# Kernel optimization log

Hardware: AMD Instinct MI355X
Metric: run time of the kernel (lower is better)

Reference implementation:

```python
import jax, jax.numpy as jnp
import numpy as np

E, TOP_K = 8, 2          # num_experts, num_experts_per_tok
B, S, H, I = 4, 2048, 1024, 4096  # batch, seq, hidden, intermediate
STD = 0.02


def setup_inputs() -> dict:
    key = jax.random.key(0)
    k0, k1, k2, k3 = jax.random.split(key, 4)
    return {
        "x": jax.random.normal(k0, (B, S, H), jnp.float32),
        "w_gate": jax.random.normal(k1, (E, H), jnp.float32) * STD,                 # gate: Linear(H->E, no bias)
        "w_fc": jax.random.normal(k2, (E, I, H), jnp.float32) * STD,                # c_fc per-expert [E, out, in]
        "b_fc": jnp.zeros((E, I), jnp.float32),
        "w_proj": jax.random.normal(k3, (E, H, I), jnp.float32) * (STD / np.sqrt(2 * 24)),  # c_proj, n_layer=24 init scale
        "b_proj": jnp.zeros((E, H), jnp.float32),
    }


def reference(x, w_gate, w_fc, b_fc, w_proj, b_proj):
    b, s, h = x.shape
    xf = x.reshape(-1, h)                       # [T, H], T = B*S
    T = xf.shape[0]

    # --- routing (softmax in fp32, top-k, renormalize) ---
    router_logits = xf @ w_gate.T               # [T, E]
    probs = jax.nn.softmax(router_logits.astype(jnp.float32), axis=-1)
    top_w, top_idx = jax.lax.top_k(probs, TOP_K)            # [T, K]
    top_w = top_w / jnp.sum(top_w, axis=-1, keepdims=True)  # normalize_expert_weights
    top_w = top_w.astype(x.dtype)

    # combine[t, e] = gate weight of expert e for token t (0 if not selected)
    combine = jnp.zeros((T, E), x.dtype).at[jnp.arange(T)[:, None], top_idx].add(top_w)

    # --- experts: weighted sum of per-expert MLPs (same math as sort/gather/scatter) ---
    out = jnp.zeros_like(xf)
    for e in range(E):
        ht = jax.nn.gelu(xf @ w_fc[e].T + b_fc[e], approximate=False)  # [T, I]
        ht = ht @ w_proj[e].T + b_proj[e]                              # [T, H]
        out = out + combine[:, e:e + 1] * ht

    return out.reshape(b, s, h), router_logits
```

## Files before the change

kernel.cpp:

```cpp
#include <hip/hip_runtime.h>
#include <hip/hip_bf16.h>
#include <math.h>

#define T_TOK 8192
#define HID 1024
#define IDIM 4096
#define NE 8
#define TK (T_TOK*2)

typedef __attribute__((ext_vector_type(8))) short short8;
typedef __attribute__((ext_vector_type(4))) float f32x4;

__global__ __launch_bounds__(256) void cvt_kernel(const float* __restrict__ src,
                                                  __hip_bfloat16* __restrict__ dst, int n4)
{
    int i = blockIdx.x * 256 + threadIdx.x;
    int stride = gridDim.x * 256;
    for (; i < n4; i += stride) {
        float4 v = ((const float4*)src)[i];
        union { __hip_bfloat16 h[4]; ushort4 u; } t;
        t.h[0] = __float2bfloat16(v.x);
        t.h[1] = __float2bfloat16(v.y);
        t.h[2] = __float2bfloat16(v.z);
        t.h[3] = __float2bfloat16(v.w);
        ((ushort4*)dst)[i] = t.u;
    }
}

__global__ __launch_bounds__(64) void router_kernel(const float* __restrict__ x,
                                                    const float* __restrict__ wg,
                                                    float* __restrict__ logits_out,
                                                    int* __restrict__ top_idx,
                                                    float* __restrict__ top_w,
                                                    int* __restrict__ counts)
{
    int t = blockIdx.x;
    int lane = threadIdx.x;
    const float* xr = x + (size_t)t * HID;
    float acc[NE];
#pragma unroll
    for (int e = 0; e < NE; e++) acc[e] = 0.f;
    for (int h = lane; h < HID; h += 64) {
        float xv = xr[h];
#pragma unroll
        for (int e = 0; e < NE; e++) acc[e] += xv * wg[e * HID + h];
    }
#pragma unroll
    for (int e = 0; e < NE; e++)
        for (int off = 32; off > 0; off >>= 1)
            acc[e] += __shfl_down(acc[e], off, 64);
    if (lane == 0) {
        float mx = acc[0];
        for (int e = 1; e < NE; e++) mx = fmaxf(mx, acc[e]);
        float p[NE]; float s = 0.f;
        for (int e = 0; e < NE; e++) { p[e] = expf(acc[e] - mx); s += p[e]; }
        for (int e = 0; e < NE; e++) logits_out[(size_t)t * NE + e] = acc[e];
        int i1 = 0;
        for (int e = 1; e < NE; e++) if (p[e] > p[i1]) i1 = e;
        int i2 = -1;
        for (int e = 0; e < NE; e++) { if (e == i1) continue; if (i2 < 0 || p[e] > p[i2]) i2 = e; }
        float w1 = p[i1], w2 = p[i2], sw = w1 + w2;
        top_idx[t * 2] = i1; top_idx[t * 2 + 1] = i2;
        top_w[t * 2] = w1 / sw; top_w[t * 2 + 1] = w2 / sw;
        atomicAdd(&counts[i1], 1);
        atomicAdd(&counts[i2], 1);
    }
}

__global__ void scan_kernel(const int* __restrict__ counts, int* __restrict__ offsets)
{
    if (threadIdx.x == 0) {
        int s = 0;
        for (int e = 0; e < NE; e++) { offsets[e] = s; s += counts[e]; }
        offsets[NE] = s;
    }
}

__global__ __launch_bounds__(256) void scatter_kernel(const int* __restrict__ top_idx,
                                                      const float* __restrict__ top_w,
                                                      const int* __restrict__ offsets,
                                                      int* __restrict__ counts2,
                                                      int* __restrict__ expert_tok,
                                                      float* __restrict__ slot_w,
                                                      int* __restrict__ slot_of)
{
    int t = blockIdx.x * 256 + threadIdx.x;
    if (t >= T_TOK) return;
    for (int k = 0; k < 2; k++) {
        int e = top_idx[t * 2 + k];
        int pos = atomicAdd(&counts2[e], 1);
        int slot = offsets[e] + pos;
        expert_tok[slot] = t;
        slot_w[slot] = top_w[t * 2 + k];
        slot_of[t * 2 + k] = slot;
    }
}

__global__ __launch_bounds__(256) void gather_kernel(const float* __restrict__ x,
                                                     const int* __restrict__ expert_tok,
                                                     __hip_bfloat16* __restrict__ xg)
{
    int slot = blockIdx.x;
    int tok = expert_tok[slot];
    const float* src = x + (size_t)tok * HID;
    __hip_bfloat16* dst = xg + (size_t)slot * HID;
    for (int h = threadIdx.x; h < HID; h += 256)
        dst[h] = __float2bfloat16(src[h]);
}

#define LDS_STRIDE 40

template <int KDIM>
__device__ __forceinline__ void moe_gemm_loop(const __hip_bfloat16* __restrict__ A,
                                              int m0, int cnt,
                                              const __hip_bfloat16* __restrict__ B,
                                              __hip_bfloat16* Alds, __hip_bfloat16* Blds,
                                              f32x4 (&acc)[4][4])
{
    const int tid = threadIdx.x;
    const int lane = tid & 63, wave = tid >> 6;
    const int wm = (wave & 1) * 64, wn = (wave >> 1) * 64;
    const int fm = lane & 15, q = lane >> 4;

    for (int kt = 0; kt < KDIM / 32; ++kt) {
        const int k0 = kt * 32;
        __syncthreads();
#pragma unroll
        for (int i = 0; i < 2; i++) {
            int cid = tid + 256 * i;
            int r = cid >> 2, c = cid & 3;
            int ra = m0 + r; ra = (ra < cnt) ? ra : (cnt - 1);
            *(uint4*)&Alds[r * LDS_STRIDE + c * 8] =
                *(const uint4*)&A[(size_t)ra * KDIM + k0 + c * 8];
            *(uint4*)&Blds[r * LDS_STRIDE + c * 8] =
                *(const uint4*)&B[(size_t)r * KDIM + k0 + c * 8];
        }
        __syncthreads();
        short8 af[4], bfr[4];
#pragma unroll
        for (int mi = 0; mi < 4; mi++)
            af[mi] = *(const short8*)&Alds[(wm + mi * 16 + fm) * LDS_STRIDE + q * 8];
#pragma unroll
        for (int ni = 0; ni < 4; ni++)
            bfr[ni] = *(const short8*)&Blds[(wn + ni * 16 + fm) * LDS_STRIDE + q * 8];
#pragma unroll
        for (int mi = 0; mi < 4; mi++)
#pragma unroll
            for (int ni = 0; ni < 4; ni++)
                acc[mi][ni] = __builtin_amdgcn_mfma_f32_16x16x32_bf16(af[mi], bfr[ni],
                                                                      acc[mi][ni], 0, 0, 0);
    }
}

__global__ __launch_bounds__(256) void gemm_fc_kernel(const __hip_bfloat16* __restrict__ xg,
                                                      const __hip_bfloat16* __restrict__ wfc,
                                                      const float* __restrict__ b_fc,
                                                      const int* __restrict__ offsets,
                                                      __hip_bfloat16* __restrict__ ht)
{
    __shared__ __hip_bfloat16 Alds[128 * LDS_STRIDE];
    __shared__ __hip_bfloat16 Blds[128 * LDS_STRIDE];
    const int e = blockIdx.z;
    const int off = offsets[e];
    const int cnt = offsets[e + 1] - off;
    const int m0 = blockIdx.y * 128;
    if (m0 >= cnt) return;
    const int n0 = blockIdx.x * 128;

    f32x4 acc[4][4] = {};
    moe_gemm_loop<HID>(xg + (size_t)off * HID, m0, cnt,
                       wfc + (size_t)e * IDIM * HID + (size_t)n0 * HID, Alds, Blds, acc);

    const int tid = threadIdx.x, lane = tid & 63, wave = tid >> 6;
    const int wm = (wave & 1) * 64, wn = (wave >> 1) * 64, fm = lane & 15, q = lane >> 4;
#pragma unroll
    for (int ni = 0; ni < 4; ni++) {
        int n = n0 + wn + ni * 16 + fm;
        float bias = b_fc[(size_t)e * IDIM + n];
#pragma unroll
        for (int mi = 0; mi < 4; mi++) {
#pragma unroll
            for (int r = 0; r < 4; r++) {
                int m = m0 + wm + mi * 16 + q * 4 + r;
                if (m < cnt) {
                    float v = acc[mi][ni][r] + bias;
                    float g = 0.5f * v * (1.0f + erff(v * 0.70710678118654752f));
                    ht[(size_t)(off + m) * IDIM + n] = __float2bfloat16(g);
                }
            }
        }
    }
}

__global__ __launch_bounds__(256) void gemm_proj_kernel(const __hip_bfloat16* __restrict__ ht,
                                                        const __hip_bfloat16* __restrict__ wproj,
                                                        const float* __restrict__ b_proj,
                                                        const int* __restrict__ offsets,
                                                        const float* __restrict__ slot_w,
                                                        __hip_bfloat16* __restrict__ contrib)
{
    __shared__ __hip_bfloat16 Alds[128 * LDS_STRIDE];
    __shared__ __hip_bfloat16 Blds[128 * LDS_STRIDE];
    const int e = blockIdx.z;
    const int off = offsets[e];
    const int cnt = offsets[e + 1] - off;
    const int m0 = blockIdx.y * 128;
    if (m0 >= cnt) return;
    const int n0 = blockIdx.x * 128;

    f32x4 acc[4][4] = {};
    moe_gemm_loop<IDIM>(ht + (size_t)off * IDIM, m0, cnt,
                        wproj + (size_t)e * HID * IDIM + (size_t)n0 * IDIM, Alds, Blds, acc);

    const int tid = threadIdx.x, lane = tid & 63, wave = tid >> 6;
    const int wm = (wave & 1) * 64, wn = (wave >> 1) * 64, fm = lane & 15, q = lane >> 4;
#pragma unroll
    for (int mi = 0; mi < 4; mi++) {
#pragma unroll
        for (int r = 0; r < 4; r++) {
            int m = m0 + wm + mi * 16 + q * 4 + r;
            if (m >= cnt) continue;
            float sw = slot_w[off + m];
#pragma unroll
            for (int ni = 0; ni < 4; ni++) {
                int n = n0 + wn + ni * 16 + fm;
                float v = acc[mi][ni][r] + b_proj[(size_t)e * HID + n];
                contrib[(size_t)(off + m) * HID + n] = __float2bfloat16(v * sw);
            }
        }
    }
}

__global__ __launch_bounds__(256) void combine_kernel(const __hip_bfloat16* __restrict__ contrib,
                                                      const int* __restrict__ slot_of,
                                                      float* __restrict__ out)
{
    int t = blockIdx.x;
    int s0 = slot_of[t * 2], s1 = slot_of[t * 2 + 1];
    const __hip_bfloat16* c0 = contrib + (size_t)s0 * HID;
    const __hip_bfloat16* c1 = contrib + (size_t)s1 * HID;
    float* o = out + (size_t)t * HID;
    for (int h = threadIdx.x; h < HID; h += 256)
        o[h] = __bfloat162float(c0[h]) + __bfloat162float(c1[h]);
}

extern "C" void kernel_launch(void* const* d_in, const int* in_sizes, int n_in,
                              void* d_out, int out_size, void* d_ws, size_t ws_size,
                              hipStream_t stream)
{
    const float* x      = (const float*)d_in[0];
    const float* w_gate = (const float*)d_in[1];
    const float* w_fc   = (const float*)d_in[2];
    const float* b_fc   = (const float*)d_in[3];
    const float* w_proj = (const float*)d_in[4];
    const float* b_proj = (const float*)d_in[5];
    float* out = (float*)d_out;
    float* logits_out = out + (size_t)T_TOK * HID;

    char* ws = (char*)d_ws;
    const size_t WB = (size_t)NE * IDIM * HID * 2;
    size_t o_wfc     = 0;
    size_t o_wproj   = o_wfc + WB;
    size_t o_xg      = o_wproj + WB;
    size_t o_ht      = o_xg + (size_t)TK * HID * 2;
    size_t o_contrib = o_ht + (size_t)TK * IDIM * 2;
    size_t o_route   = o_contrib + (size_t)TK * HID * 2;

    __hip_bfloat16* wfc_b   = (__hip_bfloat16*)(ws + o_wfc);
    __hip_bfloat16* wproj_b = (__hip_bfloat16*)(ws + o_wproj);
    __hip_bfloat16* xg      = (__hip_bfloat16*)(ws + o_xg);
    __hip_bfloat16* ht      = (__hip_bfloat16*)(ws + o_ht);
    __hip_bfloat16* contrib = (__hip_bfloat16*)(ws + o_contrib);

    size_t ro = o_route;
    int*   top_idx    = (int*)(ws + ro);   ro += (size_t)T_TOK * 2 * 4;
    float* top_w      = (float*)(ws + ro); ro += (size_t)T_TOK * 2 * 4;
    int*   counts     = (int*)(ws + ro);   ro += NE * 4;
    int*   counts2    = (int*)(ws + ro);   ro += NE * 4;
    int*   offsets    = (int*)(ws + ro);   ro += 16 * 4;
    int*   expert_tok = (int*)(ws + ro);   ro += (size_t)TK * 4;
    float* slot_w     = (float*)(ws + ro); ro += (size_t)TK * 4;
    int*   slot_of    = (int*)(ws + ro);   ro += (size_t)T_TOK * 2 * 4;

    if (ws_size < ro) return;

    hipMemsetAsync(counts, 0, 2 * NE * sizeof(int), stream);

    const int n4 = NE * IDIM * HID / 4;
    cvt_kernel<<<2048, 256, 0, stream>>>(w_fc, wfc_b, n4);
    cvt_kernel<<<2048, 256, 0, stream>>>(w_proj, wproj_b, n4);

    router_kernel<<<T_TOK, 64, 0, stream>>>(x, w_gate, logits_out, top_idx, top_w, counts);
    scan_kernel<<<1, 64, 0, stream>>>(counts, offsets);
    scatter_kernel<<<T_TOK / 256, 256, 0, stream>>>(top_idx, top_w, offsets, counts2,
                                                    expert_tok, slot_w, slot_of);
    gather_kernel<<<TK, 256, 0, stream>>>(x, expert_tok, xg);

    gemm_fc_kernel<<<dim3(IDIM / 128, T_TOK / 128, NE), 256, 0, stream>>>(
        xg, wfc_b, b_fc, offsets, ht);
    gemm_proj_kernel<<<dim3(HID / 128, T_TOK / 128, NE), 256, 0, stream>>>(
        ht, wproj_b, b_proj, offsets, slot_w, contrib);

    combine_kernel<<<T_TOK, 256, 0, stream>>>(contrib, slot_of, out);
}
```

Before: 1.207 ms.

## Load GEMM tiles with direct global-to-LDS loads and vectorize gather/combine

Replaces the register-staged global-to-LDS copy in the shared MoE GEMM loop with global_load_lds 16-byte direct loads, which removes the LDS padding (stride 40 to 32). It also vectorizes the gather and combine kernels to float4/ushort4 per thread. The aim is fewer VGPR round trips and instructions in the tile load path. The risk is LDS bank conflicts on the unpadded layout during fragment reads, and gather/combine now assume a 256-thread block covers exactly HID/4 elements.

```diff
diff --git a/kernel.cpp b/kernel.cpp
--- a/kernel.cpp
+++ b/kernel.cpp
@@ -10,6 +10,13 @@
 
 typedef __attribute__((ext_vector_type(8))) short short8;
 typedef __attribute__((ext_vector_type(4))) float f32x4;
+
+__device__ __forceinline__ void gld_lds16(const __hip_bfloat16* g, __hip_bfloat16* l)
+{
+    __builtin_amdgcn_global_load_lds(
+        (const __attribute__((address_space(1))) void*)g,
+        (__attribute__((address_space(3))) void*)l, 16, 0, 0);
+}
 
 __global__ __launch_bounds__(256) void cvt_kernel(const float* __restrict__ src,
                                                   __hip_bfloat16* __restrict__ dst, int n4)
@@ -102,13 +109,17 @@
 {
     int slot = blockIdx.x;
     int tok = expert_tok[slot];
-    const float* src = x + (size_t)tok * HID;
-    __hip_bfloat16* dst = xg + (size_t)slot * HID;
-    for (int h = threadIdx.x; h < HID; h += 256)
-        dst[h] = __float2bfloat16(src[h]);
-}
-
-#define LDS_STRIDE 40
+    const float4* src = (const float4*)(x + (size_t)tok * HID);
+    ushort4* dst = (ushort4*)(xg + (size_t)slot * HID);
+    int h = threadIdx.x;
+    float4 v = src[h];
+    union { __hip_bfloat16 h4[4]; ushort4 u; } t;
+    t.h4[0] = __float2bfloat16(v.x);
+    t.h4[1] = __float2bfloat16(v.y);
+    t.h4[2] = __float2bfloat16(v.z);
+    t.h4[3] = __float2bfloat16(v.w);
+    dst[h] = t.u;
+}
 
 template <int KDIM>
 __device__ __forceinline__ void moe_gemm_loop(const __hip_bfloat16* __restrict__ A,
@@ -122,27 +133,35 @@
     const int wm = (wave & 1) * 64, wn = (wave >> 1) * 64;
     const int fm = lane & 15, q = lane >> 4;
 
+    const int srow = wave * 32 + (lane >> 2);
+    const int schunk = (lane & 3) * 8;
+    int ra0 = m0 + srow;      ra0 = (ra0 < cnt) ? ra0 : (cnt - 1);
+    int ra1 = m0 + srow + 16; ra1 = (ra1 < cnt) ? ra1 : (cnt - 1);
+    const __hip_bfloat16* gA0 = A + (size_t)ra0 * KDIM + schunk;
+    const __hip_bfloat16* gA1 = A + (size_t)ra1 * KDIM + schunk;
+    const __hip_bfloat16* gB0 = B + (size_t)srow * KDIM + schunk;
+    const __hip_bfloat16* gB1 = B + (size_t)(srow + 16) * KDIM + schunk;
+    __hip_bfloat16* lA0 = Alds + (wave * 32) * 32;
+    __hip_bfloat16* lA1 = Alds + (wave * 32 + 16) * 32;
+    __hip_bfloat16* lB0 = Blds + (wave * 32) * 32;
+    __hip_bfloat16* lB1 = Blds + (wave * 32 + 16) * 32;
+
     for (int kt = 0; kt < KDIM / 32; ++kt) {
-        const int k0 = kt * 32;
         __syncthreads();
-#pragma unroll
-        for (int i = 0; i < 2; i++) {
-            int cid = tid + 256 * i;
-            int r = cid >> 2, c = cid & 3;
-            int ra = m0 + r; ra = (ra < cnt) ? ra : (cnt - 1);
-            *(uint4*)&Alds[r * LDS_STRIDE + c * 8] =
-                *(const uint4*)&A[(size_t)ra * KDIM + k0 + c * 8];
-            *(uint4*)&Blds[r * LDS_STRIDE + c * 8] =
-                *(const uint4*)&B[(size_t)r * KDIM + k0 + c * 8];
-        }
+        gld_lds16(gA0, lA0);
+        gld_lds16(gA1, lA1);
+        gld_lds16(gB0, lB0);
+        gld_lds16(gB1, lB1);
+        gA0 += 32; gA1 += 32; gB0 += 32; gB1 += 32;
         __syncthreads();
+
         short8 af[4], bfr[4];
 #pragma unroll
         for (int mi = 0; mi < 4; mi++)
-            af[mi] = *(const short8*)&Alds[(wm + mi * 16 + fm) * LDS_STRIDE + q * 8];
+            af[mi] = *(const short8*)&Alds[(wm + mi * 16 + fm) * 32 + q * 8];
 #pragma unroll
         for (int ni = 0; ni < 4; ni++)
-            bfr[ni] = *(const short8*)&Blds[(wn + ni * 16 + fm) * LDS_STRIDE + q * 8];
+            bfr[ni] = *(const short8*)&Blds[(wn + ni * 16 + fm) * 32 + q * 8];
 #pragma unroll
         for (int mi = 0; mi < 4; mi++)
 #pragma unroll
@@ -158,8 +177,8 @@
                                                       const int* __restrict__ offsets,
                                                       __hip_bfloat16* __restrict__ ht)
 {
-    __shared__ __hip_bfloat16 Alds[128 * LDS_STRIDE];
-    __shared__ __hip_bfloat16 Blds[128 * LDS_STRIDE];
+    __shared__ __hip_bfloat16 Alds[128 * 32];
+    __shared__ __hip_bfloat16 Blds[128 * 32];
     const int e = blockIdx.z;
     const int off = offsets[e];
     const int cnt = offsets[e + 1] - off;
@@ -199,8 +218,8 @@
                                                         const float* __restrict__ slot_w,
                                                         __hip_bfloat16* __restrict__ contrib)
 {
-    __shared__ __hip_bfloat16 Alds[128 * LDS_STRIDE];
-    __shared__ __hip_bfloat16 Blds[128 * LDS_STRIDE];
+    __shared__ __hip_bfloat16 Alds[128 * 32];
+    __shared__ __hip_bfloat16 Blds[128 * 32];
     const int e = blockIdx.z;
     const int off = offsets[e];
     const int cnt = offsets[e + 1] - off;
@@ -237,11 +256,20 @@
 {
     int t = blockIdx.x;
     int s0 = slot_of[t * 2], s1 = slot_of[t * 2 + 1];
-    const __hip_bfloat16* c0 = contrib + (size_t)s0 * HID;
-    const __hip_bfloat16* c1 = contrib + (size_t)s1 * HID;
-    float* o = out + (size_t)t * HID;
-    for (int h = threadIdx.x; h < HID; h += 256)
-        o[h] = __bfloat162float(c0[h]) + __bfloat162float(c1[h]);
+    const ushort4* c0 = (const ushort4*)(contrib + (size_t)s0 * HID);
+    const ushort4* c1 = (const ushort4*)(contrib + (size_t)s1 * HID);
+    float4* o = (float4*)(out + (size_t)t * HID);
+    int h = threadIdx.x;
+    ushort4 a = c0[h], b = c1[h];
+    union { unsigned u; float f; } f0, f1, f2, f3;
+    f0.u = ((unsigned)a.x << 16); f1.u = ((unsigned)a.y << 16);
+    f2.u = ((unsigned)a.z << 16); f3.u = ((unsigned)a.w << 16);
+    union { unsigned u; float f; } g0, g1, g2, g3;
+    g0.u = ((unsigned)b.x << 16); g1.u = ((unsigned)b.y << 16);
+    g2.u = ((unsigned)b.z << 16); g3.u = ((unsigned)b.w << 16);
+    float4 r;
+    r.x = f0.f + g0.f; r.y = f1.f + g1.f; r.z = f2.f + g2.f; r.w = f3.f + g3.f;
+    o[h] = r;
 }
 
 extern "C" void kernel_launch(void* const* d_in, const int* in_sizes, int n_in,
```

Result: faster. 1.136 ms (-5.9%).
